# Optimization experiments

Hardware: AMD Instinct MI355X
Metric: run time of the kernel (lower is better)

Reference implementation:

```python
import jax, jax.numpy as jnp
import numpy as np

F, H1, H2, K, L = 16, 64, 64, 8, 8          # n_features, hidden sizes, num_bins, num_layers
NBP = 3 * K + 1                              # num_bijector_params per feature
RMIN, RMAX = -10.0, 10.0
MIN_BIN, MIN_SLOPE = 1e-4, 1e-4              # distrax RationalQuadraticSpline defaults


def setup_inputs() -> dict:
    key = jax.random.key(0)
    ks = jax.random.split(key, 11)
    B = 131072
    return {
        "x": jax.random.normal(ks[0], (B, F), jnp.float32),
        "W0": jax.random.normal(ks[1], (L, F, F), jnp.float32) * 0.1,
        "b0": jax.random.normal(ks[2], (L, F), jnp.float32) * 0.01,
        "W1": jax.random.normal(ks[3], (L, F, H1), jnp.float32) * 0.1,
        "b1": jax.random.normal(ks[4], (L, H1), jnp.float32) * 0.01,
        "W2": jax.random.normal(ks[5], (L, H1, H2), jnp.float32) * 0.1,
        "b2": jax.random.normal(ks[6], (L, H2), jnp.float32) * 0.01,
        "Wout": jax.random.normal(ks[7], (L, H2, F * NBP), jnp.float32) * 0.05,
        "bout": jax.random.normal(ks[8], (L, F * NBP), jnp.float32) * 0.01,
        # scalar-affine coupling params; scale kept positive (init is ones in the module)
        "scale": jnp.exp(0.05 * jax.random.normal(ks[9], (L, F), jnp.float32)),
        "shift": jax.random.normal(ks[10], (L, F), jnp.float32) * 0.1,
    }


def _rq_spline_fwd(params, x):
    """distrax.RationalQuadraticSpline forward_and_log_det (elementwise).
    params: (B, F, 3K+1), x: (B, F) -> (y, log_det) each (B, F)."""
    uw, uh, ud = params[..., :K], params[..., K:2 * K], params[..., 2 * K:]
    total = RMAX - RMIN
    w = jax.nn.softmax(uw, axis=-1) * (total - K * MIN_BIN) + MIN_BIN   # bin widths
    h = jax.nn.softmax(uh, axis=-1) * (total - K * MIN_BIN) + MIN_BIN   # bin heights
    offset = float(np.log(np.expm1(1.0 - MIN_SLOPE)))                   # softplus(0+offset)=1
    d = jax.nn.softplus(ud + offset) + MIN_SLOPE                        # knot slopes (B,F,K+1)
    zeros = jnp.zeros(w.shape[:-1] + (1,), w.dtype)
    xpos = RMIN + jnp.concatenate([zeros, jnp.cumsum(w, -1)], -1)       # knot x (B,F,K+1)
    ypos = RMIN + jnp.concatenate([zeros, jnp.cumsum(h, -1)], -1)       # knot y (B,F,K+1)
    # per-element bin search
    idx = jnp.clip(jnp.sum((x[..., None] >= xpos).astype(jnp.int32), -1) - 1, 0, K - 1)
    take = lambda a: jnp.take_along_axis(a, idx[..., None], axis=-1)[..., 0]
    xk, xk1 = take(xpos[..., :-1]), take(xpos[..., 1:])
    yk, yk1 = take(ypos[..., :-1]), take(ypos[..., 1:])
    dk, dk1 = take(d[..., :-1]), take(d[..., 1:])
    bw = xk1 - xk
    bh = yk1 - yk
    s = bh / bw                                                          # bin slope
    z = jnp.clip((x - xk) / bw, 0.0, 1.0)
    z1m = 1.0 - z
    den = s + (dk1 + dk - 2.0 * s) * z * z1m
    y = yk + bh * (s * z * z + dk * z * z1m) / den
    num_ld = dk1 * z * z + 2.0 * s * z * z1m + dk * z1m * z1m
    ld = 2.0 * jnp.log(s) + jnp.log(num_ld) - 2.0 * jnp.log(den)
    outside = (x <= RMIN) | (x >= RMAX)                                  # identity outside range
    return jnp.where(outside, x, y), jnp.where(outside, 0.0, ld)


def reference(x, W0, b0, W1, b1, W2, b2, Wout, bout, scale, shift):
    """log_prob of Transformed(base, Inverse(Chain(layers))) == base.log_prob(Chain.fwd(x)) + fwd logdet."""
    B = x.shape[0]
    feat = jnp.arange(F)
    z = x
    logdet = jnp.zeros((B,), x.dtype)
    # distrax.Chain applies the last-appended layer first -> iterate layers in reverse;
    # within layer i: spline coupling (appended second) then scalar-affine coupling.
    for i in reversed(range(L)):
        mask = ((feat + i) % 2).astype(bool)        # True = pass-through / conditioner input
        mz = jnp.where(mask, z, 0.0)
        hid = jnp.tanh(mz @ W0[i] + b0[i])
        hid = jnp.tanh(hid @ W1[i] + b1[i])
        hid = hid @ W2[i] + b2[i]                   # last MLP layer is linear
        p = (hid @ Wout[i] + bout[i]).reshape(B, F, NBP)
        y, ld = _rq_spline_fwd(p, z)
        z = jnp.where(mask, z, y)
        logdet = logdet + jnp.sum(jnp.where(mask, 0.0, ld), axis=-1)
        # scalar affine coupling with all-False mask: transforms every feature
        z = z * scale[i] + shift[i]
        logdet = logdet + jnp.sum(jnp.log(jnp.abs(scale[i])))
    base_lp = -0.5 * jnp.sum(z * z, axis=-1) - 0.5 * F * float(np.log(2.0 * np.pi))
    return base_lp + logdet
```

## Files before the change

kernel.cpp:

```cpp
#include <hip/hip_runtime.h>
#include <math.h>

typedef _Float16 f16;
typedef _Float16 half8 __attribute__((ext_vector_type(8)));
typedef float f32x16 __attribute__((ext_vector_type(16)));

#define DEV __device__ __forceinline__

#define W1F_OFF 0
#define W2F_OFF 16384
#define WOF_OFF 81920
#define BOF_OFF 344064
#define SUMLOG_OFF 352256

#define H0_OFF    0
#define H0_STRIDE 48
#define H_OFF     12288
#define H_STRIDE  144
#define P_OFF     49152
#define P_STRIDE  116
#define LDS_BYTES 78848

DEV float frcp(float x){ return __builtin_amdgcn_rcpf(x); }
DEV float fexp(float x){ return __expf(x); }
DEV float flog(float x){ return __logf(x); }

DEV float ftanh(float x){
  float e = fexp(2.f * x);
  float r = frcp(e + 1.f);
  return fmaf(-2.f, r, 1.f);
}

DEV void rq_spline(const float p[25], float xv, float &y_out, float &ld_out)
{
  float ew[8]; float sw = 0.f;
#pragma unroll
  for (int k = 0; k < 8; ++k){ ew[k] = fexp(p[k]); sw += ew[k]; }
  float rw = frcp(sw) * 19.9992f;

  float xpos[9];
  xpos[0] = -10.f;
#pragma unroll
  for (int k = 0; k < 8; ++k) xpos[k + 1] = xpos[k] + fmaf(ew[k], rw, 1e-4f);

  int idx = 0;
#pragma unroll
  for (int j = 1; j < 8; ++j) idx += (xv >= xpos[j]) ? 1 : 0;

  float xk = xpos[0], ewk = ew[0];
#pragma unroll
  for (int j = 1; j < 8; ++j){
    bool sel = (idx >= j);
    xk  = sel ? xpos[j] : xk;
    ewk = sel ? ew[j]   : ewk;
  }
  float bw = fmaf(ewk, rw, 1e-4f);

  float eh[8]; float shs = 0.f;
#pragma unroll
  for (int k = 0; k < 8; ++k){ eh[k] = fexp(p[8 + k]); shs += eh[k]; }
  float rh = frcp(shs) * 19.9992f;

  float S = 0.f, ehk = eh[0];
#pragma unroll
  for (int k = 1; k < 8; ++k){
    bool sel = (idx >= k);
    S   += sel ? eh[k - 1] : 0.f;
    ehk  = sel ? eh[k]     : ehk;
  }
  float yk = fmaf(S, rh, fmaf((float)idx, 1e-4f, -10.f));
  float bh = fmaf(ehk, rh, 1e-4f);

  float uA = p[16], uB = p[17];
#pragma unroll
  for (int j = 1; j < 8; ++j){
    bool sel = (idx >= j);
    uA = sel ? p[16 + j] : uA;
    uB = sel ? p[17 + j] : uB;
  }
  float vA = uA + 0.54116666f;
  float dk  = fmaxf(vA, 0.f) + flog(1.f + fexp(-fabsf(vA))) + 1e-4f;
  float vB = uB + 0.54116666f;
  float dk1 = fmaxf(vB, 0.f) + flog(1.f + fexp(-fabsf(vB))) + 1e-4f;

  float rbw = frcp(bw);
  float s   = bh * rbw;
  float zf  = fminf(fmaxf((xv - xk) * rbw, 0.f), 1.f);
  float z1  = 1.f - zf;
  float zz  = zf * zf, z01 = zf * z1;
  float den = s + (dk1 + dk - 2.f * s) * z01;
  float rden = frcp(den);
  float yv  = yk + bh * (s * zz + dk * z01) * rden;
  float num = dk1 * zz + 2.f * s * z01 + dk * z1 * z1;
  float ldv = flog(s * s * num * rden * rden);

  bool outside = (xv <= -10.f) || (xv >= 10.f);
  y_out  = outside ? xv : yv;
  ld_out = outside ? 0.f : ldv;
}

extern "C" __global__ void __launch_bounds__(256)
prep_kernel(const float* __restrict__ W1, const float* __restrict__ W2,
            const float* __restrict__ Wo, const float* __restrict__ bout,
            const float* __restrict__ scale, char* __restrict__ ws)
{
  int tid = blockIdx.x * 256 + threadIdx.x;
  if (tid < 1024){
    int fi = tid >> 6, lane = tid & 63;
    int l = fi >> 1, nt = fi & 1;
    int n = nt * 32 + (lane & 31), khi = lane >> 5;
    half8 h;
#pragma unroll
    for (int j = 0; j < 8; ++j){ int k = khi * 8 + j; h[j] = (f16)W1[l * 1024 + k * 64 + n]; }
    *(half8*)(ws + W1F_OFF + fi * 1024 + lane * 16) = h;
  } else if (tid < 5120){
    int idx = tid - 1024;
    int fi = idx >> 6, lane = idx & 63;
    int l = fi >> 3, kt = (fi >> 1) & 3, nt = fi & 1;
    int n = nt * 32 + (lane & 31), khi = lane >> 5;
    half8 h;
#pragma unroll
    for (int j = 0; j < 8; ++j){ int k = kt * 16 + khi * 8 + j; h[j] = (f16)W2[l * 4096 + k * 64 + n]; }
    *(half8*)(ws + W2F_OFF + fi * 1024 + lane * 16) = h;
  } else if (tid < 21504){
    int idx = tid - 5120;
    int fi = idx >> 6, lane = idx & 63;
    int l = fi >> 5, u = (fi >> 2) & 7, kt = fi & 3;
    int f = (l & 1) + 2 * u;
    int c = lane & 31, khi = lane >> 5;
    half8 h;
#pragma unroll
    for (int j = 0; j < 8; ++j){
      int k = kt * 16 + khi * 8 + j;
      float v = (c < 25) ? Wo[l * 25600 + k * 400 + f * 25 + c] : 0.f;
      h[j] = (f16)v;
    }
    *(half8*)(ws + WOF_OFF + fi * 1024 + lane * 16) = h;
  } else if (tid < 23552){
    int idx = tid - 21504;
    int l = idx >> 8, u = (idx >> 5) & 7, c = idx & 31;
    int f = (l & 1) + 2 * u;
    float v = (c < 25) ? bout[l * 400 + f * 25 + c] : 0.f;
    ((float*)(ws + BOF_OFF))[idx] = v;
  } else if (tid == 23552){
    float acc = 0.f;
    for (int i = 0; i < 128; ++i) acc += logf(fabsf(scale[i]));
    *(float*)(ws + SUMLOG_OFF) = acc;
  }
}

template<int PAR>
DEV void layer_mfma(int l,
                    const float* __restrict__ W0, const float* __restrict__ b0,
                    const float* __restrict__ b1v, const float* __restrict__ b2v,
                    const float* __restrict__ scv, const float* __restrict__ shv,
                    const char* __restrict__ ws, char* lds,
                    float (&z)[16], float &logdet,
                    int t, int lane, int wv, int ln31, int khi)
{
  const float* w0  = W0 + l * 256;
  const float* bb0 = b0 + l * 16;
  const int rowbase = khi * 4;

  const half8* W1F = (const half8*)(ws + W1F_OFF);
  const half8* W2F = (const half8*)(ws + W2F_OFF);
  half8 w1f[2];
#pragma unroll
  for (int nt = 0; nt < 2; ++nt) w1f[nt] = W1F[(l * 2 + nt) * 64 + lane];
  half8 w2f[8];
#pragma unroll
  for (int kt = 0; kt < 4; ++kt)
#pragma unroll
    for (int nt = 0; nt < 2; ++nt)
      w2f[kt * 2 + nt] = W2F[((l * 4 + kt) * 2 + nt) * 64 + lane];
  float bias1[2], bias2[2];
#pragma unroll
  for (int nt = 0; nt < 2; ++nt){
    bias1[nt] = b1v[l * 64 + nt * 32 + ln31];
    bias2[nt] = b2v[l * 64 + nt * 32 + ln31];
  }

  float h0[16];
#pragma unroll
  for (int j = 0; j < 16; ++j) h0[j] = bb0[j];
#pragma unroll
  for (int u = 0; u < 8; ++u){
    const int f = (1 - PAR) + 2 * u;
    const float v = z[f];
#pragma unroll
    for (int j = 0; j < 16; ++j) h0[j] = fmaf(v, w0[f * 16 + j], h0[j]);
  }
  {
    half8 lo, hi;
#pragma unroll
    for (int j = 0; j < 8; ++j){ lo[j] = (f16)ftanh(h0[j]); hi[j] = (f16)ftanh(h0[8 + j]); }
    *(half8*)(lds + H0_OFF + t * H0_STRIDE)      = lo;
    *(half8*)(lds + H0_OFF + t * H0_STRIDE + 16) = hi;
  }

  half8 a0[2];
#pragma unroll
  for (int mt = 0; mt < 2; ++mt){
    int s = wv * 64 + mt * 32 + ln31;
    a0[mt] = *(const half8*)(lds + H0_OFF + s * H0_STRIDE + khi * 16);
  }
  f32x16 d1[2][2];
#pragma unroll
  for (int mt = 0; mt < 2; ++mt)
#pragma unroll
    for (int nt = 0; nt < 2; ++nt)
#pragma unroll
      for (int i = 0; i < 16; ++i) d1[mt][nt][i] = bias1[nt];
#pragma unroll
  for (int nt = 0; nt < 2; ++nt)
#pragma unroll
    for (int mt = 0; mt < 2; ++mt)
      d1[mt][nt] = __builtin_amdgcn_mfma_f32_32x32x16_f16(a0[mt], w1f[nt], d1[mt][nt], 0, 0, 0);
#pragma unroll
  for (int mt = 0; mt < 2; ++mt)
#pragma unroll
    for (int nt = 0; nt < 2; ++nt)
#pragma unroll
      for (int i = 0; i < 16; ++i){
        int row = (i & 3) + 8 * (i >> 2) + rowbase;
        int s = wv * 64 + mt * 32 + row;
        float v = ftanh(d1[mt][nt][i]);
        *(f16*)(lds + H_OFF + s * H_STRIDE + (nt * 32 + ln31) * 2) = (f16)v;
      }

  half8 a1[2][4];
#pragma unroll
  for (int mt = 0; mt < 2; ++mt){
    int s = wv * 64 + mt * 32 + ln31;
#pragma unroll
    for (int kt = 0; kt < 4; ++kt)
      a1[mt][kt] = *(const half8*)(lds + H_OFF + s * H_STRIDE + kt * 32 + khi * 16);
  }
  f32x16 d2[2][2];
#pragma unroll
  for (int mt = 0; mt < 2; ++mt)
#pragma unroll
    for (int nt = 0; nt < 2; ++nt)
#pragma unroll
      for (int i = 0; i < 16; ++i) d2[mt][nt][i] = bias2[nt];
#pragma unroll
  for (int kt = 0; kt < 4; ++kt)
#pragma unroll
    for (int nt = 0; nt < 2; ++nt)
#pragma unroll
      for (int mt = 0; mt < 2; ++mt)
        d2[mt][nt] = __builtin_amdgcn_mfma_f32_32x32x16_f16(a1[mt][kt], w2f[kt * 2 + nt], d2[mt][nt], 0, 0, 0);

  const half8* WOF = (const half8*)(ws + WOF_OFF);
  const float* BOF = (const float*)(ws + BOF_OFF);
  half8 bfn[4];
#pragma unroll
  for (int kt = 0; kt < 4; ++kt) bfn[kt] = WOF[((l * 8 + 0) * 4 + kt) * 64 + lane];
  float biasn = BOF[(l * 8 + 0) * 32 + ln31];

#pragma unroll
  for (int mt = 0; mt < 2; ++mt)
#pragma unroll
    for (int nt = 0; nt < 2; ++nt)
#pragma unroll
      for (int i = 0; i < 16; ++i){
        int row = (i & 3) + 8 * (i >> 2) + rowbase;
        int s = wv * 64 + mt * 32 + row;
        float v = d2[mt][nt][i];
        *(f16*)(lds + H_OFF + s * H_STRIDE + (nt * 32 + ln31) * 2) = (f16)v;
      }

  half8 a2[2][4];
#pragma unroll
  for (int mt = 0; mt < 2; ++mt){
    int s = wv * 64 + mt * 32 + ln31;
#pragma unroll
    for (int kt = 0; kt < 4; ++kt)
      a2[mt][kt] = *(const half8*)(lds + H_OFF + s * H_STRIDE + kt * 32 + khi * 16);
  }

  {
    f32x16 dp[2];
#pragma unroll
    for (int mt = 0; mt < 2; ++mt)
#pragma unroll
      for (int i = 0; i < 16; ++i) dp[mt][i] = biasn;
#pragma unroll
    for (int kt = 0; kt < 4; ++kt)
#pragma unroll
      for (int mt = 0; mt < 2; ++mt)
        dp[mt] = __builtin_amdgcn_mfma_f32_32x32x16_f16(a2[mt][kt], bfn[kt], dp[mt], 0, 0, 0);
    if (ln31 < 25){
#pragma unroll
      for (int mt = 0; mt < 2; ++mt)
#pragma unroll
        for (int i = 0; i < 16; ++i){
          int row = (i & 3) + 8 * (i >> 2) + rowbase;
          int s = wv * 64 + mt * 32 + row;
          *(float*)(lds + P_OFF + s * P_STRIDE + ln31 * 4) = dp[mt][i];
        }
    }
  }
#pragma unroll
  for (int kt = 0; kt < 4; ++kt) bfn[kt] = WOF[((l * 8 + 1) * 4 + kt) * 64 + lane];
  biasn = BOF[(l * 8 + 1) * 32 + ln31];

#pragma unroll 1
  for (int u = 0; u < 8; ++u){
    float p[25];
#pragma unroll
    for (int j = 0; j < 25; ++j)
      p[j] = *(const float*)(lds + P_OFF + t * P_STRIDE + j * 4);

    if (u < 7){
      f32x16 dp[2];
#pragma unroll
      for (int mt = 0; mt < 2; ++mt)
#pragma unroll
        for (int i = 0; i < 16; ++i) dp[mt][i] = biasn;
#pragma unroll
      for (int kt = 0; kt < 4; ++kt)
#pragma unroll
        for (int mt = 0; mt < 2; ++mt)
          dp[mt] = __builtin_amdgcn_mfma_f32_32x32x16_f16(a2[mt][kt], bfn[kt], dp[mt], 0, 0, 0);
      if (ln31 < 25){
#pragma unroll
        for (int mt = 0; mt < 2; ++mt)
#pragma unroll
          for (int i = 0; i < 16; ++i){
            int row = (i & 3) + 8 * (i >> 2) + rowbase;
            int s = wv * 64 + mt * 32 + row;
            *(float*)(lds + P_OFF + s * P_STRIDE + ln31 * 4) = dp[mt][i];
          }
      }
      if (u < 6){
#pragma unroll
        for (int kt = 0; kt < 4; ++kt) bfn[kt] = WOF[((l * 8 + u + 2) * 4 + kt) * 64 + lane];
        biasn = BOF[(l * 8 + u + 2) * 32 + ln31];
      }
    }

    const int f = PAR + 2 * u;
    float y, ld;
    rq_spline(p, z[f], y, ld);
    z[f] = y;
    logdet += ld;
  }

  const float* scp = scv + l * 16;
  const float* shp = shv + l * 16;
#pragma unroll
  for (int j = 0; j < 16; ++j)
    z[j] = fmaf(z[j], scp[j], shp[j]);
}

extern "C" __global__ void __launch_bounds__(256, 2)
flow_kernel(const float* __restrict__ x,
            const float* __restrict__ W0, const float* __restrict__ b0,
            const float* __restrict__ b1v, const float* __restrict__ b2v,
            const float* __restrict__ scv, const float* __restrict__ shv,
            const char* __restrict__ ws, float* __restrict__ out, int B)
{
  extern __shared__ char lds[];
  const int t    = threadIdx.x;
  const int lane = t & 63;
  const int wv   = t >> 6;
  const int ln31 = lane & 31;
  const int khi  = lane >> 5;
  const int g    = blockIdx.x * 256 + t;

  float z[16];
  const float4* xv = reinterpret_cast<const float4*>(x + (size_t)g * 16);
  float4 a0 = xv[0], a1 = xv[1], a2 = xv[2], a3 = xv[3];
  z[0]=a0.x; z[1]=a0.y; z[2]=a0.z; z[3]=a0.w;
  z[4]=a1.x; z[5]=a1.y; z[6]=a1.z; z[7]=a1.w;
  z[8]=a2.x; z[9]=a2.y; z[10]=a2.z; z[11]=a2.w;
  z[12]=a3.x; z[13]=a3.y; z[14]=a3.z; z[15]=a3.w;

  float logdet = 0.f;
  for (int l = 7; l >= 0; --l){
    if (l & 1) layer_mfma<1>(l, W0, b0, b1v, b2v, scv, shv, ws, lds, z, logdet, t, lane, wv, ln31, khi);
    else       layer_mfma<0>(l, W0, b0, b1v, b2v, scv, shv, ws, lds, z, logdet, t, lane, wv, ln31, khi);
  }

  float sumlog = *(const float*)(ws + SUMLOG_OFF);
  float ss = 0.f;
#pragma unroll
  for (int j = 0; j < 16; ++j) ss = fmaf(z[j], z[j], ss);
  out[g] = -0.5f * ss - 14.7030165f + logdet + sumlog;
}

extern "C" void kernel_launch(void* const* d_in, const int* in_sizes, int n_in,
                              void* d_out, int out_size, void* d_ws, size_t ws_size,
                              hipStream_t stream)
{
  const float* x    = (const float*)d_in[0];
  const float* W0   = (const float*)d_in[1];
  const float* b0   = (const float*)d_in[2];
  const float* W1   = (const float*)d_in[3];
  const float* b1   = (const float*)d_in[4];
  const float* W2   = (const float*)d_in[5];
  const float* b2   = (const float*)d_in[6];
  const float* Wout = (const float*)d_in[7];
  const float* bout = (const float*)d_in[8];
  const float* scale= (const float*)d_in[9];
  const float* shift= (const float*)d_in[10];

  int B = in_sizes[0] / 16;

  hipLaunchKernelGGL(prep_kernel, dim3(93), dim3(256), 0, stream,
                     W1, W2, Wout, bout, scale, (char*)d_ws);

  hipLaunchKernelGGL(flow_kernel, dim3(B / 256), dim3(256), LDS_BYTES, stream,
                     x, W0, b0, b1, b2, scale, shift,
                     (const char*)d_ws, (float*)d_out, B);
}
```

Measured before the change: 211.0 us.

## Interleave spline width/height params for packed math and double-buffer param tiles

Output-projection weights and biases are permuted at pack time so width and height logits sit side by side. This lets the spline compute both softmaxes, knot positions and bin sizes with two-wide vector math, and it derives the bin height from knot differences instead of a separate masked prefix sum. The per-feature loop is unrolled by two with separate register buffers. The MFMA for the next feature's parameters is issued before the current spline is evaluated, which overlaps matrix work with the transcendental-heavy spline math. The extra parameter buffers raise register pressure under the 2-blocks launch bound and may cause spills.

```diff
diff --git a/kernel.cpp b/kernel.cpp
--- a/kernel.cpp
+++ b/kernel.cpp
@@ -4,6 +4,7 @@
 typedef _Float16 f16;
 typedef _Float16 half8 __attribute__((ext_vector_type(8)));
 typedef float f32x16 __attribute__((ext_vector_type(16)));
+typedef float f32x2  __attribute__((ext_vector_type(2)));
 
 #define DEV __device__ __forceinline__
 
@@ -13,13 +14,15 @@
 #define BOF_OFF 344064
 #define SUMLOG_OFF 352256
 
+#define PIDX(c) ((c) < 16 ? (((c) >> 1) + (((c) & 1) << 3)) : (c))
+
 #define H0_OFF    0
 #define H0_STRIDE 48
 #define H_OFF     12288
 #define H_STRIDE  144
 #define P_OFF     49152
-#define P_STRIDE  116
-#define LDS_BYTES 78848
+#define P_STRIDE  120
+#define LDS_BYTES 79872
 
 DEV float frcp(float x){ return __builtin_amdgcn_rcpf(x); }
 DEV float fexp(float x){ return __expf(x); }
@@ -31,45 +34,43 @@
   return fmaf(-2.f, r, 1.f);
 }
 
-DEV void rq_spline(const float p[25], float xv, float &y_out, float &ld_out)
-{
-  float ew[8]; float sw = 0.f;
-#pragma unroll
-  for (int k = 0; k < 8; ++k){ ew[k] = fexp(p[k]); sw += ew[k]; }
-  float rw = frcp(sw) * 19.9992f;
-
-  float xpos[9];
-  xpos[0] = -10.f;
-#pragma unroll
-  for (int k = 0; k < 8; ++k) xpos[k + 1] = xpos[k] + fmaf(ew[k], rw, 1e-4f);
+DEV void rq_spline(const float p[26], float xv, float &y_out, float &ld_out)
+{
+  f32x2 e[8];
+  f32x2 sum = {0.f, 0.f};
+#pragma unroll
+  for (int k = 0; k < 8; ++k){
+    f32x2 wh = {p[2*k], p[2*k+1]};
+    f32x2 tt = wh * 1.44269504f;
+    e[k].x = exp2f(tt.x);
+    e[k].y = exp2f(tt.y);
+    sum += e[k];
+  }
+  f32x2 rr; rr.x = frcp(sum.x); rr.y = frcp(sum.y);
+  rr *= 19.9992f;
+
+  f32x2 pos[9];
+  pos[0].x = -10.f; pos[0].y = -10.f;
+#pragma unroll
+  for (int k = 0; k < 8; ++k){
+    f32x2 tt = pos[k] + 1e-4f;
+    pos[k+1] = e[k] * rr + tt;
+  }
 
   int idx = 0;
 #pragma unroll
-  for (int j = 1; j < 8; ++j) idx += (xv >= xpos[j]) ? 1 : 0;
-
-  float xk = xpos[0], ewk = ew[0];
+  for (int j = 1; j < 8; ++j) idx += (xv >= pos[j].x) ? 1 : 0;
+
+  f32x2 kn0 = pos[0], kn1 = pos[1];
 #pragma unroll
   for (int j = 1; j < 8; ++j){
     bool sel = (idx >= j);
-    xk  = sel ? xpos[j] : xk;
-    ewk = sel ? ew[j]   : ewk;
-  }
-  float bw = fmaf(ewk, rw, 1e-4f);
-
-  float eh[8]; float shs = 0.f;
-#pragma unroll
-  for (int k = 0; k < 8; ++k){ eh[k] = fexp(p[8 + k]); shs += eh[k]; }
-  float rh = frcp(shs) * 19.9992f;
-
-  float S = 0.f, ehk = eh[0];
-#pragma unroll
-  for (int k = 1; k < 8; ++k){
-    bool sel = (idx >= k);
-    S   += sel ? eh[k - 1] : 0.f;
-    ehk  = sel ? eh[k]     : ehk;
-  }
-  float yk = fmaf(S, rh, fmaf((float)idx, 1e-4f, -10.f));
-  float bh = fmaf(ehk, rh, 1e-4f);
+    kn0 = sel ? pos[j]     : kn0;
+    kn1 = sel ? pos[j + 1] : kn1;
+  }
+  f32x2 bwh = kn1 - kn0;
+  float xk = kn0.x, yk = kn0.y;
+  float bw = bwh.x, bh = bwh.y;
 
   float uA = p[16], uB = p[17];
 #pragma unroll
@@ -132,7 +133,7 @@
 #pragma unroll
     for (int j = 0; j < 8; ++j){
       int k = kt * 16 + khi * 8 + j;
-      float v = (c < 25) ? Wo[l * 25600 + k * 400 + f * 25 + c] : 0.f;
+      float v = (c < 25) ? Wo[l * 25600 + k * 400 + f * 25 + PIDX(c)] : 0.f;
       h[j] = (f16)v;
     }
     *(half8*)(ws + WOF_OFF + fi * 1024 + lane * 16) = h;
@@ -140,12 +141,40 @@
     int idx = tid - 21504;
     int l = idx >> 8, u = (idx >> 5) & 7, c = idx & 31;
     int f = (l & 1) + 2 * u;
-    float v = (c < 25) ? bout[l * 400 + f * 25 + c] : 0.f;
+    float v = (c < 25) ? bout[l * 400 + f * 25 + PIDX(c)] : 0.f;
     ((float*)(ws + BOF_OFF))[idx] = v;
   } else if (tid == 23552){
     float acc = 0.f;
     for (int i = 0; i < 128; ++i) acc += logf(fabsf(scale[i]));
     *(float*)(ws + SUMLOG_OFF) = acc;
+  }
+}
+
+DEV void produce_p(const half8 bf[4], float bias, const half8 a2[2][4],
+                   char* lds, const char* pbase,
+                   int ln31, int wv, int rowbase, float* pout)
+{
+  f32x16 dp0, dp1;
+#pragma unroll
+  for (int i = 0; i < 16; ++i){ dp0[i] = bias; dp1[i] = bias; }
+#pragma unroll
+  for (int kt = 0; kt < 4; ++kt){
+    dp0 = __builtin_amdgcn_mfma_f32_32x32x16_f16(a2[0][kt], bf[kt], dp0, 0, 0, 0);
+    dp1 = __builtin_amdgcn_mfma_f32_32x32x16_f16(a2[1][kt], bf[kt], dp1, 0, 0, 0);
+  }
+  if (ln31 < 25){
+#pragma unroll
+    for (int i = 0; i < 16; ++i){
+      int row = (i & 3) + 8 * (i >> 2) + rowbase;
+      int s0 = wv * 64 + row;
+      *(float*)(lds + P_OFF + s0 * P_STRIDE + ln31 * 4) = dp0[i];
+      *(float*)(lds + P_OFF + (s0 + 32) * P_STRIDE + ln31 * 4) = dp1[i];
+    }
+  }
+#pragma unroll
+  for (int j = 0; j < 13; ++j){
+    f32x2 v = *(const f32x2*)(pbase + 8 * j);
+    pout[2*j] = v.x; pout[2*j+1] = v.y;
   }
 }
 
@@ -161,6 +190,7 @@
   const float* w0  = W0 + l * 256;
   const float* bb0 = b0 + l * 16;
   const int rowbase = khi * 4;
+  const char* pbase = lds + P_OFF + t * P_STRIDE;
 
   const half8* W1F = (const half8*)(ws + W1F_OFF);
   const half8* W2F = (const half8*)(ws + W2F_OFF);
@@ -253,10 +283,11 @@
 
   const half8* WOF = (const half8*)(ws + WOF_OFF);
   const float* BOF = (const float*)(ws + BOF_OFF);
-  half8 bfn[4];
-#pragma unroll
-  for (int kt = 0; kt < 4; ++kt) bfn[kt] = WOF[((l * 8 + 0) * 4 + kt) * 64 + lane];
-  float biasn = BOF[(l * 8 + 0) * 32 + ln31];
+  half8 bfa[4], bfb[4];
+  float ba, bb;
+#pragma unroll
+  for (int kt = 0; kt < 4; ++kt) bfa[kt] = WOF[((l * 8 + 0) * 4 + kt) * 64 + lane];
+  ba = BOF[(l * 8 + 0) * 32 + ln31];
 
 #pragma unroll
   for (int mt = 0; mt < 2; ++mt)
@@ -266,8 +297,7 @@
       for (int i = 0; i < 16; ++i){
         int row = (i & 3) + 8 * (i >> 2) + rowbase;
         int s = wv * 64 + mt * 32 + row;
-        float v = d2[mt][nt][i];
-        *(f16*)(lds + H_OFF + s * H_STRIDE + (nt * 32 + ln31) * 2) = (f16)v;
+        *(f16*)(lds + H_OFF + s * H_STRIDE + (nt * 32 + ln31) * 2) = (f16)d2[mt][nt][i];
       }
 
   half8 a2[2][4];
@@ -279,72 +309,38 @@
       a2[mt][kt] = *(const half8*)(lds + H_OFF + s * H_STRIDE + kt * 32 + khi * 16);
   }
 
-  {
-    f32x16 dp[2];
-#pragma unroll
-    for (int mt = 0; mt < 2; ++mt)
-#pragma unroll
-      for (int i = 0; i < 16; ++i) dp[mt][i] = biasn;
-#pragma unroll
-    for (int kt = 0; kt < 4; ++kt)
-#pragma unroll
-      for (int mt = 0; mt < 2; ++mt)
-        dp[mt] = __builtin_amdgcn_mfma_f32_32x32x16_f16(a2[mt][kt], bfn[kt], dp[mt], 0, 0, 0);
-    if (ln31 < 25){
-#pragma unroll
-      for (int mt = 0; mt < 2; ++mt)
-#pragma unroll
-        for (int i = 0; i < 16; ++i){
-          int row = (i & 3) + 8 * (i >> 2) + rowbase;
-          int s = wv * 64 + mt * 32 + row;
-          *(float*)(lds + P_OFF + s * P_STRIDE + ln31 * 4) = dp[mt][i];
-        }
-    }
-  }
-#pragma unroll
-  for (int kt = 0; kt < 4; ++kt) bfn[kt] = WOF[((l * 8 + 1) * 4 + kt) * 64 + lane];
-  biasn = BOF[(l * 8 + 1) * 32 + ln31];
+  float pA[26], pB[26];
+  produce_p(bfa, ba, a2, lds, pbase, ln31, wv, rowbase, pA);
+#pragma unroll
+  for (int kt = 0; kt < 4; ++kt) bfb[kt] = WOF[((l * 8 + 1) * 4 + kt) * 64 + lane];
+  bb = BOF[(l * 8 + 1) * 32 + ln31];
 
 #pragma unroll 1
-  for (int u = 0; u < 8; ++u){
-    float p[25];
-#pragma unroll
-    for (int j = 0; j < 25; ++j)
-      p[j] = *(const float*)(lds + P_OFF + t * P_STRIDE + j * 4);
-
-    if (u < 7){
-      f32x16 dp[2];
-#pragma unroll
-      for (int mt = 0; mt < 2; ++mt)
-#pragma unroll
-        for (int i = 0; i < 16; ++i) dp[mt][i] = biasn;
-#pragma unroll
-      for (int kt = 0; kt < 4; ++kt)
-#pragma unroll
-        for (int mt = 0; mt < 2; ++mt)
-          dp[mt] = __builtin_amdgcn_mfma_f32_32x32x16_f16(a2[mt][kt], bfn[kt], dp[mt], 0, 0, 0);
-      if (ln31 < 25){
-#pragma unroll
-        for (int mt = 0; mt < 2; ++mt)
-#pragma unroll
-          for (int i = 0; i < 16; ++i){
-            int row = (i & 3) + 8 * (i >> 2) + rowbase;
-            int s = wv * 64 + mt * 32 + row;
-            *(float*)(lds + P_OFF + s * P_STRIDE + ln31 * 4) = dp[mt][i];
-          }
-      }
-      if (u < 6){
-#pragma unroll
-        for (int kt = 0; kt < 4; ++kt) bfn[kt] = WOF[((l * 8 + u + 2) * 4 + kt) * 64 + lane];
-        biasn = BOF[(l * 8 + u + 2) * 32 + ln31];
-      }
-    }
-
-    const int f = PAR + 2 * u;
-    float y, ld;
-    rq_spline(p, z[f], y, ld);
-    z[f] = y;
-    logdet += ld;
+  for (int u = 0; u < 8; u += 2){
+    produce_p(bfb, bb, a2, lds, pbase, ln31, wv, rowbase, pB);
+    if (u < 6){
+#pragma unroll
+      for (int kt = 0; kt < 4; ++kt) bfa[kt] = WOF[((l * 8 + u + 2) * 4 + kt) * 64 + lane];
+      ba = BOF[(l * 8 + u + 2) * 32 + ln31];
+    }
+    {
+      float y, ld;
+      rq_spline(pA, z[PAR + 2 * u], y, ld);
+      z[PAR + 2 * u] = y;
+      logdet += ld;
+    }
+    if (u < 6){
+      produce_p(bfa, ba, a2, lds, pbase, ln31, wv, rowbase, pA);
+#pragma unroll
+      for (int kt = 0; kt < 4; ++kt) bfb[kt] = WOF[((l * 8 + u + 3) * 4 + kt) * 64 + lane];
+      bb = BOF[(l * 8 + u + 3) * 32 + ln31];
+    }
+    {
+      float y, ld;
+      rq_spline(pB, z[PAR + 2 * u + 2 - 1 + 1], y, ld);
+      z[PAR + 2 * (u + 1)] = y;
+      logdet += ld;
+    }
   }
 
   const float* scp = scv + l * 16;
```

Result: slower. 228.9 us (+8.5%).
